# Optimization experiments

Measured on AMD Instinct MI355X. Metric: run time of the kernel, lower is better.

## Reference

```python
import jax, jax.numpy as jnp
import numpy as np

EPS = 1e-5

def sage_conv(x, edge_index, w_l, b_l, w_r):
    # PyG SAGEConv with mean aggregation: lin_l(mean of source-neighbor feats per dst) + lin_r(x)
    n = x.shape[0]
    src, dst = edge_index[0], edge_index[1]
    agg = jax.ops.segment_sum(x[src], dst, num_segments=n)  # [N, d]
    deg = jax.ops.segment_sum(jnp.ones((edge_index.shape[1],), x.dtype), dst, num_segments=n)
    agg = agg / jnp.maximum(deg, 1.0)[:, None]
    return agg @ w_l + b_l + x @ w_r

def batchnorm_eval(x, gamma, beta, mean, var):
    return (x - mean) * (gamma * jax.lax.rsqrt(var + EPS)) + beta

def setup_inputs() -> dict:
    key = jax.random.key(0)
    ks = jax.random.split(key, 12)
    N, E, D, H, O = 10000, 160000, 512, 512, 256
    inp = {
        'x': jax.random.normal(ks[0], (N, D), jnp.float32),
        'edge_index': jax.random.randint(ks[1], (2, E), 0, N, jnp.int32),
        'w_l1': jax.random.normal(ks[2], (D, H), jnp.float32) * (1.0 / np.sqrt(D)),
        'b1': jnp.zeros((H,), jnp.float32),
        'w_r1': jax.random.normal(ks[3], (D, H), jnp.float32) * (1.0 / np.sqrt(D)),
        'bn1_gamma': jnp.ones((H,), jnp.float32),
        'bn1_beta': jnp.zeros((H,), jnp.float32),
        'bn1_mean': jax.random.normal(ks[4], (H,), jnp.float32) * 0.1,
        'bn1_var': jax.random.uniform(ks[5], (H,), jnp.float32, 0.5, 1.5),
        'w_l2': jax.random.normal(ks[6], (H, H), jnp.float32) * (1.0 / np.sqrt(H)),
        'b2': jnp.zeros((H,), jnp.float32),
        'w_r2': jax.random.normal(ks[7], (H, H), jnp.float32) * (1.0 / np.sqrt(H)),
        'bn2_gamma': jnp.ones((H,), jnp.float32),
        'bn2_beta': jnp.zeros((H,), jnp.float32),
        'bn2_mean': jax.random.normal(ks[8], (H,), jnp.float32) * 0.1,
        'bn2_var': jax.random.uniform(ks[9], (H,), jnp.float32, 0.5, 1.5),
        'w_l3': jax.random.normal(ks[10], (H, O), jnp.float32) * (1.0 / np.sqrt(H)),
        'b3': jnp.zeros((O,), jnp.float32),
        'w_r3': jax.random.normal(ks[11], (H, O), jnp.float32) * (1.0 / np.sqrt(H)),
    }
    return inp

def reference(x, edge_index, w_l1, b1, w_r1, bn1_gamma, bn1_beta, bn1_mean, bn1_var,
              w_l2, b2, w_r2, bn2_gamma, bn2_beta, bn2_mean, bn2_var,
              w_l3, b3, w_r3):
    # Layer 1: SAGEConv -> BN (eval) -> ReLU (dropout is identity in eval)
    h = sage_conv(x, edge_index, w_l1, b1, w_r1)
    h = jax.nn.relu(batchnorm_eval(h, bn1_gamma, bn1_beta, bn1_mean, bn1_var))
    # Layer 2
    h = sage_conv(h, edge_index, w_l2, b2, w_r2)
    h = jax.nn.relu(batchnorm_eval(h, bn2_gamma, bn2_beta, bn2_mean, bn2_var))
    # Layer 3 (no BN/ReLU)
    return sage_conv(h, edge_index, w_l3, b3, w_r3)
```

## Files before the change

### kernel.cpp

```cpp
#include <hip/hip_runtime.h>

#define NNODE 10000
#define NEDGE 160000

using frag8 = __attribute__((ext_vector_type(8))) short;
using f32x4 = __attribute__((ext_vector_type(4))) float;

__device__ __forceinline__ unsigned short f2bf(float f) {
    union { float f; unsigned u; } v; v.f = f;
    unsigned r = (v.u + 0x7fffu + ((v.u >> 16) & 1u)) >> 16;
    return (unsigned short)r;
}
__device__ __forceinline__ float bf2f(unsigned short s) {
    union { unsigned u; float f; } v; v.u = ((unsigned)s) << 16; return v.f;
}

__global__ void k_count(const int* __restrict__ dst, int E, int* __restrict__ deg) {
    int e = blockIdx.x * 256 + threadIdx.x;
    if (e < E) atomicAdd(&deg[dst[e]], 1);
}

__global__ __launch_bounds__(1024) void k_scan(const int* __restrict__ deg,
                                               int* __restrict__ rs,
                                               int* __restrict__ cur, int n, int total) {
    const int tid = threadIdx.x;
    const int CH = 10;
    const int base = tid * CH;
    int vals[CH];
    int tsum = 0;
#pragma unroll
    for (int j = 0; j < CH; j++) {
        int v = (base + j < n) ? deg[base + j] : 0;
        vals[j] = v; tsum += v;
    }
    const int lane = tid & 63, wid = tid >> 6;
    int x = tsum;
#pragma unroll
    for (int d = 1; d < 64; d <<= 1) {
        int y = __shfl_up(x, d, 64);
        if (lane >= d) x += y;
    }
    __shared__ int wt[16];
    if (lane == 63) wt[wid] = x;
    __syncthreads();
    if (tid == 0) {
        int c = 0;
#pragma unroll
        for (int k = 0; k < 16; k++) { int t = wt[k]; wt[k] = c; c += t; }
    }
    __syncthreads();
    int run = wt[wid] + x - tsum;
#pragma unroll
    for (int j = 0; j < CH; j++) {
        if (base + j < n) { rs[base + j] = run; cur[base + j] = run; }
        run += vals[j];
    }
    if (tid == 0) rs[n] = total;
}

__global__ void k_fill(const int* __restrict__ src, const int* __restrict__ dst,
                       int E, int* __restrict__ cur, int* __restrict__ csr) {
    int e = blockIdx.x * 256 + threadIdx.x;
    if (e < E) {
        int p = atomicAdd(&cur[dst[e]], 1);
        csr[p] = src[e];
    }
}

__global__ __launch_bounds__(256) void k_prep(
    const float* __restrict__ x, unsigned short* __restrict__ xb,
    const float* __restrict__ wl1, const float* __restrict__ wr1,
    const float* __restrict__ wl2, const float* __restrict__ wr2,
    const float* __restrict__ wl3, const float* __restrict__ wr3,
    unsigned short* __restrict__ bt1, unsigned short* __restrict__ bt2,
    unsigned short* __restrict__ bt3,
    const float* __restrict__ b1, const float* __restrict__ g1, const float* __restrict__ be1,
    const float* __restrict__ m1, const float* __restrict__ v1,
    const float* __restrict__ b2, const float* __restrict__ g2, const float* __restrict__ be2,
    const float* __restrict__ m2, const float* __restrict__ v2,
    const float* __restrict__ b3,
    float* __restrict__ sc1, float* __restrict__ sh1,
    float* __restrict__ sc2, float* __restrict__ sh2,
    float* __restrict__ sc3, float* __restrict__ sh3) {
    const int b = blockIdx.x, tid = threadIdx.x;
    if (b < 5000) {
        int i = b * 256 + tid;
        float4 f = ((const float4*)x)[i];
        ushort4 o;
        o.x = f2bf(f.x); o.y = f2bf(f.y); o.z = f2bf(f.z); o.w = f2bf(f.w);
        ((ushort4*)xb)[i] = o;
        return;
    }
    if (b == 6280) {
        for (int t = tid; t < 512; t += 256) {
            float s1 = g1[t] * rsqrtf(v1[t] + 1e-5f);
            sc1[t] = s1; sh1[t] = (b1[t] - m1[t]) * s1 + be1[t];
            float s2 = g2[t] * rsqrtf(v2[t] + 1e-5f);
            sc2[t] = s2; sh2[t] = (b2[t] - m2[t]) * s2 + be2[t];
        }
        if (tid < 256) { sc3[tid] = 1.0f; sh3[tid] = b3[tid]; }
        return;
    }
    __shared__ float t[32][33];
    int tj = b - 5000;
    const float* srcp; unsigned short* dstp; int C, koff, ntilesN;
    if (tj < 1024) {
        int job = tj >> 8; int tile = tj & 255; C = 512; ntilesN = 16;
        srcp = (job == 0) ? wl1 : (job == 1) ? wr1 : (job == 2) ? wl2 : wr2;
        dstp = (job < 2) ? bt1 : bt2; koff = (job & 1) * 512;
        tj = tile;
    } else {
        int jj = tj - 1024; int job = jj >> 7; int tile = jj & 127; C = 256; ntilesN = 8;
        srcp = (job == 0) ? wl3 : wr3; dstp = bt3; koff = job * 512;
        tj = tile;
    }
    int k0 = (tj / ntilesN) * 32, c0 = (tj % ntilesN) * 32;
    int tx = tid & 31, ty = tid >> 5;
#pragma unroll
    for (int q = 0; q < 4; q++)
        t[ty + 8 * q][tx] = srcp[(long)(k0 + ty + 8 * q) * C + c0 + tx];
    __syncthreads();
#pragma unroll
    for (int q = 0; q < 4; q++)
        dstp[(long)(c0 + ty + 8 * q) * 1024 + koff + k0 + tx] = f2bf(t[tx][ty + 8 * q]);
}

__global__ __launch_bounds__(64) void k_agg(const unsigned short* __restrict__ S,
                                            const int* __restrict__ rs, const int* __restrict__ csr,
                                            unsigned short* __restrict__ outb) {
    const int n = blockIdx.x;
    const int c = blockIdx.y * 128 + threadIdx.x * 2;
    const int s = rs[n], e = rs[n + 1];
    float a0 = 0.f, a1 = 0.f;
    int i = s;
    for (; i + 4 <= e; i += 4) {
        int r0 = csr[i], r1 = csr[i + 1], r2 = csr[i + 2], r3 = csr[i + 3];
        unsigned u0 = *(const unsigned*)(S + (long)r0 * 512 + c);
        unsigned u1 = *(const unsigned*)(S + (long)r1 * 512 + c);
        unsigned u2 = *(const unsigned*)(S + (long)r2 * 512 + c);
        unsigned u3 = *(const unsigned*)(S + (long)r3 * 512 + c);
        a0 += bf2f((unsigned short)(u0 & 0xffffu)); a1 += bf2f((unsigned short)(u0 >> 16));
        a0 += bf2f((unsigned short)(u1 & 0xffffu)); a1 += bf2f((unsigned short)(u1 >> 16));
        a0 += bf2f((unsigned short)(u2 & 0xffffu)); a1 += bf2f((unsigned short)(u2 >> 16));
        a0 += bf2f((unsigned short)(u3 & 0xffffu)); a1 += bf2f((unsigned short)(u3 >> 16));
    }
    for (; i < e; i++) {
        unsigned u = *(const unsigned*)(S + (long)csr[i] * 512 + c);
        a0 += bf2f((unsigned short)(u & 0xffffu)); a1 += bf2f((unsigned short)(u >> 16));
    }
    const int cnt = e - s;
    const float inv = 1.f / (float)(cnt > 1 ? cnt : 1);
    unsigned o = (unsigned)f2bf(a0 * inv) | ((unsigned)f2bf(a1 * inv) << 16);
    *(unsigned*)(outb + (long)n * 512 + c) = o;
}

template <int MODE, int NOUT>
__global__ __launch_bounds__(256) void k_gemm(const unsigned short* __restrict__ Agg,
                                              const unsigned short* __restrict__ Self,
                                              const unsigned short* __restrict__ Bt,
                                              const float* __restrict__ sc, const float* __restrict__ sh,
                                              unsigned short* __restrict__ hout, float* __restrict__ fout,
                                              int M) {
    __shared__ __align__(16) short As[128 * 64];
    __shared__ __align__(16) short Bs[64 * 64];
    const int tid = threadIdx.x;
    const int m0 = blockIdx.x * 128, n0 = blockIdx.y * 64;
    const int w = tid >> 6, lane = tid & 63;
    const int wm = (w >> 1) * 64, wn = (w & 1) * 32;
    const int fr = lane & 15;
    const int fq = lane >> 4;
    const int sw = fr & 7;

    const int srow = w * 8 + (lane >> 3);
    const int scol = (((lane & 7) ^ (lane >> 3)) * 8);
    short* asDst = As + w * 8 * 64;
    short* bsDst = Bs + w * 8 * 64;

    f32x4 acc[4][2];
#pragma unroll
    for (int i = 0; i < 4; i++)
#pragma unroll
        for (int j = 0; j < 2; j++)
#pragma unroll
            for (int r = 0; r < 4; r++) acc[i][j][r] = 0.f;

    for (int k0 = 0; k0 < 1024; k0 += 64) {
        const short* abase = (const short*)((k0 < 512) ? Agg : Self);
        const int kk = k0 & 511;
        __syncthreads();
#pragma unroll
        for (int cch = 0; cch < 4; cch++)
            __builtin_amdgcn_global_load_lds(
                (const __attribute__((address_space(1))) void*)(abase + (long)(m0 + cch * 32 + srow) * 512 + kk + scol),
                (__attribute__((address_space(3))) void*)(asDst + cch * 32 * 64), 16, 0, 0);
#pragma unroll
        for (int cch = 0; cch < 2; cch++)
            __builtin_amdgcn_global_load_lds(
                (const __attribute__((address_space(1))) void*)((const short*)Bt + (long)(n0 + cch * 32 + srow) * 1024 + k0 + scol),
                (__attribute__((address_space(3))) void*)(bsDst + cch * 32 * 64), 16, 0, 0);
        __syncthreads();
#pragma unroll
        for (int ks = 0; ks < 2; ks++) {
            frag8 af[4], bf[2];
#pragma unroll
            for (int i = 0; i < 4; i++)
                af[i] = *(const frag8*)(As + (wm + i * 16 + fr) * 64 + (((ks * 4 + fq) ^ sw) * 8));
#pragma unroll
            for (int j = 0; j < 2; j++)
                bf[j] = *(const frag8*)(Bs + (wn + j * 16 + fr) * 64 + (((ks * 4 + fq) ^ sw) * 8));
#pragma unroll
            for (int i = 0; i < 4; i++)
#pragma unroll
                for (int j = 0; j < 2; j++)
                    acc[i][j] = __builtin_amdgcn_mfma_f32_16x16x32_bf16(af[i], bf[j], acc[i][j], 0, 0, 0);
        }
    }

    float scj[2], shj[2];
#pragma unroll
    for (int j = 0; j < 2; j++) {
        int col = n0 + wn + j * 16 + fr;
        scj[j] = sc[col]; shj[j] = sh[col];
    }
#pragma unroll
    for (int i = 0; i < 4; i++) {
        int rowb = m0 + wm + i * 16 + fq * 4;
#pragma unroll
        for (int j = 0; j < 2; j++) {
            int col = n0 + wn + j * 16 + fr;
#pragma unroll
            for (int r = 0; r < 4; r++) {
                int row = rowb + r;
                if (row < M) {
                    float y = acc[i][j][r] * scj[j] + shj[j];
                    if constexpr (MODE == 0) {
                        y = fmaxf(y, 0.f);
                        hout[(long)row * 512 + col] = f2bf(y);
                    } else {
                        fout[(long)row * NOUT + col] = y;
                    }
                }
            }
        }
    }
}

extern "C" void kernel_launch(void* const* d_in, const int* in_sizes, int n_in,
                              void* d_out, int out_size, void* d_ws, size_t ws_size,
                              hipStream_t stream) {
    const float* x    = (const float*)d_in[0];
    const int*   ei   = (const int*)d_in[1];
    const float* w_l1 = (const float*)d_in[2];
    const float* b1   = (const float*)d_in[3];
    const float* w_r1 = (const float*)d_in[4];
    const float* g1   = (const float*)d_in[5];
    const float* be1  = (const float*)d_in[6];
    const float* m1   = (const float*)d_in[7];
    const float* v1   = (const float*)d_in[8];
    const float* w_l2 = (const float*)d_in[9];
    const float* b2   = (const float*)d_in[10];
    const float* w_r2 = (const float*)d_in[11];
    const float* g2   = (const float*)d_in[12];
    const float* be2  = (const float*)d_in[13];
    const float* m2   = (const float*)d_in[14];
    const float* v2   = (const float*)d_in[15];
    const float* w_l3 = (const float*)d_in[16];
    const float* b3   = (const float*)d_in[17];
    const float* w_r3 = (const float*)d_in[18];
    float* out = (float*)d_out;

    const int N = NNODE, E = NEDGE;
    const int* srcI = ei;
    const int* dstI = ei + E;

    char* w = (char*)d_ws;
    auto alloc = [&](size_t bytes) { void* p = (void*)w; w += (bytes + 255) & ~(size_t)255; return p; };
    int* deg = (int*)alloc((size_t)N * 4);
    int* rs  = (int*)alloc((size_t)(N + 1) * 4);
    int* cur = (int*)alloc((size_t)N * 4);
    int* csr = (int*)alloc((size_t)E * 4);
    unsigned short* xb   = (unsigned short*)alloc((size_t)N * 512 * 2);
    unsigned short* bt1  = (unsigned short*)alloc((size_t)512 * 1024 * 2);
    unsigned short* bt2  = (unsigned short*)alloc((size_t)512 * 1024 * 2);
    unsigned short* bt3  = (unsigned short*)alloc((size_t)256 * 1024 * 2);
    float* sc1 = (float*)alloc(512 * 4); float* sh1 = (float*)alloc(512 * 4);
    float* sc2 = (float*)alloc(512 * 4); float* sh2 = (float*)alloc(512 * 4);
    float* sc3 = (float*)alloc(256 * 4); float* sh3 = (float*)alloc(256 * 4);
    unsigned short* agg_a = (unsigned short*)alloc((size_t)N * 512 * 2);
    unsigned short* h1    = (unsigned short*)alloc((size_t)N * 512 * 2);
    unsigned short* h2    = (unsigned short*)alloc((size_t)N * 512 * 2);
    (void)alloc(256 * 1024);

    hipMemsetAsync(deg, 0, (size_t)N * 4, stream);
    k_count<<<(E + 255) / 256, 256, 0, stream>>>(dstI, E, deg);
    k_scan<<<1, 1024, 0, stream>>>(deg, rs, cur, N, E);
    k_fill<<<(E + 255) / 256, 256, 0, stream>>>(srcI, dstI, E, cur, csr);
    k_prep<<<6281, 256, 0, stream>>>(x, xb, w_l1, w_r1, w_l2, w_r2, w_l3, w_r3,
                                     bt1, bt2, bt3,
                                     b1, g1, be1, m1, v1, b2, g2, be2, m2, v2, b3,
                                     sc1, sh1, sc2, sh2, sc3, sh3);

    dim3 g12((N + 127) / 128, 8);
    dim3 g3((N + 127) / 128, 4);
    dim3 ga(N, 4);

    k_agg<<<ga, 64, 0, stream>>>(xb, rs, csr, agg_a);
    k_gemm<0, 512><<<g12, 256, 0, stream>>>(agg_a, xb, bt1, sc1, sh1, h1, nullptr, N);
    k_agg<<<ga, 64, 0, stream>>>(h1, rs, csr, agg_a);
    k_gemm<0, 512><<<g12, 256, 0, stream>>>(agg_a, h1, bt2, sc2, sh2, h2, nullptr, N);
    k_agg<<<ga, 64, 0, stream>>>(h2, rs, csr, agg_a);
    k_gemm<1, 256><<<g3, 256, 0, stream>>>(agg_a, h2, bt3, sc3, sh3, nullptr, out, N);
}
```

Baseline: 275.9 us.

## Double-buffer GEMM LDS tiles and fold degree counting into prep kernel

The GEMM kernel now keeps two LDS buffers for the A and B tiles and issues the global-to-LDS loads for the next k-step before computing the current one, so memory latency can overlap with MFMA work. It adds a second barrier per iteration and doubles the LDS footprint, which may reduce occupancy. Separately, the edge-degree atomic counting moves into extra blocks of the prep kernel, which now runs before the scan, removing one kernel launch.

```diff
diff --git a/kernel.cpp b/kernel.cpp
--- a/kernel.cpp
+++ b/kernel.cpp
@@ -13,11 +13,6 @@
 }
 __device__ __forceinline__ float bf2f(unsigned short s) {
     union { unsigned u; float f; } v; v.u = ((unsigned)s) << 16; return v.f;
-}
-
-__global__ void k_count(const int* __restrict__ dst, int E, int* __restrict__ deg) {
-    int e = blockIdx.x * 256 + threadIdx.x;
-    if (e < E) atomicAdd(&deg[dst[e]], 1);
 }
 
 __global__ __launch_bounds__(1024) void k_scan(const int* __restrict__ deg,
@@ -81,7 +76,8 @@
     const float* __restrict__ b3,
     float* __restrict__ sc1, float* __restrict__ sh1,
     float* __restrict__ sc2, float* __restrict__ sh2,
-    float* __restrict__ sc3, float* __restrict__ sh3) {
+    float* __restrict__ sc3, float* __restrict__ sh3,
+    const int* __restrict__ dstI, int* __restrict__ deg) {
     const int b = blockIdx.x, tid = threadIdx.x;
     if (b < 5000) {
         int i = b * 256 + tid;
@@ -89,6 +85,11 @@
         ushort4 o;
         o.x = f2bf(f.x); o.y = f2bf(f.y); o.z = f2bf(f.z); o.w = f2bf(f.w);
         ((ushort4*)xb)[i] = o;
+        return;
+    }
+    if (b >= 6281) {
+        int e = (b - 6281) * 256 + tid;
+        if (e < NEDGE) atomicAdd(&deg[dstI[e]], 1);
         return;
     }
     if (b == 6280) {
@@ -161,8 +162,8 @@
                                               const float* __restrict__ sc, const float* __restrict__ sh,
                                               unsigned short* __restrict__ hout, float* __restrict__ fout,
                                               int M) {
-    __shared__ __align__(16) short As[128 * 64];
-    __shared__ __align__(16) short Bs[64 * 64];
+    __shared__ __align__(16) short As[2][128 * 64];
+    __shared__ __align__(16) short Bs[2][64 * 64];
     const int tid = threadIdx.x;
     const int m0 = blockIdx.x * 128, n0 = blockIdx.y * 64;
     const int w = tid >> 6, lane = tid & 63;
@@ -173,8 +174,7 @@
 
     const int srow = w * 8 + (lane >> 3);
     const int scol = (((lane & 7) ^ (lane >> 3)) * 8);
-    short* asDst = As + w * 8 * 64;
-    short* bsDst = Bs + w * 8 * 64;
+    const int ldsOff = w * 8 * 64;
 
     f32x4 acc[4][2];
 #pragma unroll
@@ -184,36 +184,44 @@
 #pragma unroll
             for (int r = 0; r < 4; r++) acc[i][j][r] = 0.f;
 
-    for (int k0 = 0; k0 < 1024; k0 += 64) {
-        const short* abase = (const short*)((k0 < 512) ? Agg : Self);
-        const int kk = k0 & 511;
-        __syncthreads();
+    auto issue = [&](int t, int buf) {
+        const short* abase = (const short*)((t < 8) ? Agg : Self);
+        const int kk = (t & 7) * 64;
+        const int k0 = t * 64;
 #pragma unroll
         for (int cch = 0; cch < 4; cch++)
             __builtin_amdgcn_global_load_lds(
                 (const __attribute__((address_space(1))) void*)(abase + (long)(m0 + cch * 32 + srow) * 512 + kk + scol),
-                (__attribute__((address_space(3))) void*)(asDst + cch * 32 * 64), 16, 0, 0);
+                (__attribute__((address_space(3))) void*)(&As[buf][ldsOff + cch * 32 * 64]), 16, 0, 0);
 #pragma unroll
         for (int cch = 0; cch < 2; cch++)
             __builtin_amdgcn_global_load_lds(
                 (const __attribute__((address_space(1))) void*)((const short*)Bt + (long)(n0 + cch * 32 + srow) * 1024 + k0 + scol),
-                (__attribute__((address_space(3))) void*)(bsDst + cch * 32 * 64), 16, 0, 0);
+                (__attribute__((address_space(3))) void*)(&Bs[buf][ldsOff + cch * 32 * 64]), 16, 0, 0);
+    };
+
+    issue(0, 0);
+#pragma unroll
+    for (int t = 0; t < 16; t++) {
+        const int cur = t & 1;
         __syncthreads();
+        if (t < 15) issue(t + 1, cur ^ 1);
 #pragma unroll
         for (int ks = 0; ks < 2; ks++) {
             frag8 af[4], bf[2];
 #pragma unroll
             for (int i = 0; i < 4; i++)
-                af[i] = *(const frag8*)(As + (wm + i * 16 + fr) * 64 + (((ks * 4 + fq) ^ sw) * 8));
+                af[i] = *(const frag8*)(&As[cur][(wm + i * 16 + fr) * 64 + (((ks * 4 + fq) ^ sw) * 8)]);
 #pragma unroll
             for (int j = 0; j < 2; j++)
-                bf[j] = *(const frag8*)(Bs + (wn + j * 16 + fr) * 64 + (((ks * 4 + fq) ^ sw) * 8));
+                bf[j] = *(const frag8*)(&Bs[cur][(wn + j * 16 + fr) * 64 + (((ks * 4 + fq) ^ sw) * 8)]);
 #pragma unroll
             for (int i = 0; i < 4; i++)
 #pragma unroll
                 for (int j = 0; j < 2; j++)
                     acc[i][j] = __builtin_amdgcn_mfma_f32_16x16x32_bf16(af[i], bf[j], acc[i][j], 0, 0, 0);
         }
+        __syncthreads();
     }
 
     float scj[2], shj[2];
@@ -292,13 +300,12 @@
     (void)alloc(256 * 1024);
 
     hipMemsetAsync(deg, 0, (size_t)N * 4, stream);
-    k_count<<<(E + 255) / 256, 256, 0, stream>>>(dstI, E, deg);
+    k_prep<<<6906, 256, 0, stream>>>(x, xb, w_l1, w_r1, w_l2, w_r2, w_l3, w_r3,
+                                     bt1, bt2, bt3,
+                                     b1, g1, be1, m1, v1, b2, g2, be2, m2, v2, b3,
+                                     sc1, sh1, sc2, sh2, sc3, sh3, dstI, deg);
     k_scan<<<1, 1024, 0, stream>>>(deg, rs, cur, N, E);
     k_fill<<<(E + 255) / 256, 256, 0, stream>>>(srcI, dstI, E, cur, csr);
-    k_prep<<<6281, 256, 0, stream>>>(x, xb, w_l1, w_r1, w_l2, w_r2, w_l3, w_r3,
-                                     bt1, bt2, bt3,
-                                     b1, g1, be1, m1, v1, b2, g2, be2, m2, v2, b3,
-                                     sc1, sh1, sc2, sh2, sc3, sh3);
 
     dim3 g12((N + 127) / 128, 8);
     dim3 g3((N + 127) / 128, 4);
```

Measured after the change: 272.5 us. About the same (-1.2%).
